# Kernel optimization log

Hardware: AMD Instinct MI355X
Metric: run time of the kernel (lower is better)

Reference implementation:

```python
import jax, jax.numpy as jnp
import numpy as np
from jax import lax

B, C, T, H, W = 4, 3, 2, 64, 64
DIM, HEADS, DH, MLP, DEPTH, SR, RES = 192, 3, 64, 768, 2, 2, 64
INNER = HEADS * DH  # 192 == DIM
N = RES * RES + 1   # 4097 tokens (cls + patches)


def setup_inputs() -> dict:
    key = jax.random.key(0)
    ks = iter(jax.random.split(key, 64))
    def rn(shape, s=0.02):
        return jax.random.normal(next(ks), shape, jnp.float32) * s
    d = {}
    d["x"] = jax.random.normal(next(ks), (B, C, T, H, W), jnp.float32)
    # patch embed conv3d (kernel (1,1,1) since patch_size=1) + layernorm
    d["pe_w"] = rn((DIM, C, 1, 1, 1))
    d["pe_b"] = jnp.zeros((DIM,), jnp.float32)
    d["pe_ln_g"] = jnp.ones((DIM,), jnp.float32)
    d["pe_ln_b"] = jnp.zeros((DIM,), jnp.float32)
    d["pos_emb"] = rn((1, T, N, DIM), 1.0)      # torch.randn
    d["space_token"] = rn((1, 1, DIM), 1.0)     # torch.randn
    ones2 = jnp.ones((DEPTH, DIM), jnp.float32)
    zeros2 = jnp.zeros((DEPTH, DIM), jnp.float32)
    # space transformer (Sattention with SR conv)
    d["s_ln1_g"], d["s_ln1_b"] = ones2, zeros2
    d["s_wq"] = rn((DEPTH, INNER, DIM))
    d["s_wkv"] = rn((DEPTH, 2 * INNER, DIM))
    d["s_wo"] = rn((DEPTH, DIM, INNER))
    d["s_bo"] = jnp.zeros((DEPTH, DIM), jnp.float32)
    d["s_sr_w"] = rn((DEPTH, DIM, DIM, SR, SR))
    d["s_sr_b"] = jnp.zeros((DEPTH, DIM), jnp.float32)
    d["s_ln2_g"], d["s_ln2_b"] = ones2, zeros2
    d["s_w1"] = rn((DEPTH, MLP, DIM))
    d["s_b1"] = jnp.zeros((DEPTH, MLP), jnp.float32)
    d["s_w2"] = rn((DEPTH, DIM, MLP))
    d["s_b2"] = jnp.zeros((DEPTH, DIM), jnp.float32)
    d["s_lnf_g"] = jnp.ones((DIM,), jnp.float32)
    d["s_lnf_b"] = jnp.zeros((DIM,), jnp.float32)
    # temporal transformer (plain attention over t=2 cls tokens)
    d["t_ln1_g"], d["t_ln1_b"] = ones2, zeros2
    d["t_wqkv"] = rn((DEPTH, 3 * INNER, DIM))
    d["t_wo"] = rn((DEPTH, DIM, INNER))
    d["t_bo"] = jnp.zeros((DEPTH, DIM), jnp.float32)
    d["t_ln2_g"], d["t_ln2_b"] = ones2, zeros2
    d["t_w1"] = rn((DEPTH, MLP, DIM))
    d["t_b1"] = jnp.zeros((DEPTH, MLP), jnp.float32)
    d["t_w2"] = rn((DEPTH, DIM, MLP))
    d["t_b2"] = jnp.zeros((DEPTH, DIM), jnp.float32)
    d["t_lnf_g"] = jnp.ones((DIM,), jnp.float32)
    d["t_lnf_b"] = jnp.zeros((DIM,), jnp.float32)
    return d


def _ln(x, g, b, eps=1e-5):
    m = jnp.mean(x, -1, keepdims=True)
    v = jnp.var(x, -1, keepdims=True)
    return (x - m) * lax.rsqrt(v + eps) * g + b


def _heads(t):
    b, n, _ = t.shape
    return t.reshape(b, n, HEADS, DH).transpose(0, 2, 1, 3)  # b h n d


def _attend(q, k, v):
    dots = jnp.einsum('bhid,bhjd->bhij', q, k) * (DH ** -0.5)
    attn = jax.nn.softmax(dots, axis=-1)
    o = jnp.einsum('bhij,bhjd->bhid', attn, v)
    return o.transpose(0, 2, 1, 3).reshape(q.shape[0], q.shape[2], INNER)


def _ff(x, w1, b1, w2, b2):
    h = jax.nn.gelu(x @ w1.T + b1, approximate=False)
    return h @ w2.T + b2


def _sattn(x, wq, wkv, wo, bo, srw, srb):
    bn = x.shape[0]
    q = _heads(x @ wq.T)
    # spatial reduction of non-cls tokens: b n d -> b d h w, conv stride SR
    xs = x[:, 1:].transpose(0, 2, 1).reshape(bn, DIM, RES, RES)
    xs = lax.conv_general_dilated(xs, srw, (SR, SR), 'VALID',
                                  dimension_numbers=('NCHW', 'OIHW', 'NCHW'))
    xs = xs + srb[None, :, None, None]
    xs = xs.reshape(bn, DIM, -1).transpose(0, 2, 1)
    xk = jnp.concatenate([x[:, :1], xs], axis=1)   # prepend cls token
    kv = xk @ wkv.T
    k, v = _heads(kv[..., :INNER]), _heads(kv[..., INNER:])
    return _attend(q, k, v) @ wo.T + bo


def _attn(x, wqkv, wo, bo):
    qkv = x @ wqkv.T
    q = _heads(qkv[..., :INNER])
    k = _heads(qkv[..., INNER:2 * INNER])
    v = _heads(qkv[..., 2 * INNER:])
    return _attend(q, k, v) @ wo.T + bo


def reference(x, pe_w, pe_b, pe_ln_g, pe_ln_b, pos_emb, space_token,
              s_ln1_g, s_ln1_b, s_wq, s_wkv, s_wo, s_bo, s_sr_w, s_sr_b,
              s_ln2_g, s_ln2_b, s_w1, s_b1, s_w2, s_b2, s_lnf_g, s_lnf_b,
              t_ln1_g, t_ln1_b, t_wqkv, t_wo, t_bo, t_ln2_g, t_ln2_b,
              t_w1, t_b1, t_w2, t_b2, t_lnf_g, t_lnf_b):
    # patch embed: (b,c,t,h,w) -> (b,t,hw,dim) with layernorm
    y = lax.conv_general_dilated(x, pe_w, (1, 1, 1), 'VALID',
                                 dimension_numbers=('NCDHW', 'OIDHW', 'NCDHW'))
    y = y + pe_b[None, :, None, None, None]
    y = jnp.transpose(y, (0, 2, 3, 4, 1)).reshape(B, T, RES * RES, DIM)
    y = _ln(y, pe_ln_g, pe_ln_b)
    cls = jnp.broadcast_to(space_token[:, None], (B, T, 1, DIM))
    xx = jnp.concatenate([cls, y], axis=2) + pos_emb[:, :, :N]
    xx = xx.reshape(B * T, N, DIM)
    for i in range(DEPTH):
        xx = _sattn(_ln(xx, s_ln1_g[i], s_ln1_b[i]), s_wq[i], s_wkv[i],
                    s_wo[i], s_bo[i], s_sr_w[i], s_sr_b[i]) + xx
        xx = _ff(_ln(xx, s_ln2_g[i], s_ln2_b[i]), s_w1[i], s_b1[i],
                 s_w2[i], s_b2[i]) + xx
    xx = _ln(xx, s_lnf_g, s_lnf_b)
    out = xx[:, 1:].reshape(B, T, RES, RES, DIM)
    z = xx[:, 0].reshape(B, T, DIM)
    for i in range(DEPTH):
        z = _attn(_ln(z, t_ln1_g[i], t_ln1_b[i]), t_wqkv[i], t_wo[i], t_bo[i]) + z
        z = _ff(_ln(z, t_ln2_g[i], t_ln2_b[i]), t_w1[i], t_b1[i], t_w2[i], t_b2[i]) + z
    z = _ln(z, t_lnf_g, t_lnf_b)
    return out + out * z[:, :, None, None, :]
```

## Files before the change

kernel.cpp:

```cpp
#include <hip/hip_runtime.h>
#include <hip/hip_bf16.h>
#include <math.h>

typedef __hip_bfloat16 bf16;
typedef short bf16x8 __attribute__((ext_vector_type(8)));
typedef float f32x4  __attribute__((ext_vector_type(4)));

#define BATCH 4
#define TT 2
#define BT 8
#define DIM 192
#define NTOK 4097
#define NKTOK 1025
#define HEADS 3
#define DH 64
#define MLPD 768
#define RES 64

__device__ __forceinline__ float b2f(bf16 v) { return __bfloat162float(v); }

__device__ __forceinline__ float rload(const void* p, size_t i, int flag) {
    if (flag) return __bfloat162float(((const bf16*)p)[i]);
    return ((const float*)p)[i];
}

__device__ __forceinline__ void unpack8(uint4 u, float* f) {
    unsigned w[4] = {u.x, u.y, u.z, u.w};
    #pragma unroll
    for (int k = 0; k < 4; ++k) {
        union { unsigned u; float f; } a, b;
        a.u = (w[k] & 0xFFFFu) << 16;
        b.u = w[k] & 0xFFFF0000u;
        f[2 * k] = a.f;
        f[2 * k + 1] = b.f;
    }
}

__device__ __forceinline__ void wload8(const void* W, size_t i, int flag, float* f) {
    if (flag) {
        uint4 u = *reinterpret_cast<const uint4*>((const bf16*)W + i);
        unpack8(u, f);
    } else {
        const float* p = (const float*)W + i;
        #pragma unroll
        for (int j = 0; j < 8; ++j) f[j] = p[j];
    }
}

__global__ void detect_kernel(const void* probe, int* flag) {
    unsigned u = *(const unsigned*)probe;
    *flag = (u == 0x3F800000u) ? 0 : 1;
}

__global__ __launch_bounds__(256) void patch_embed4_kernel(
        const void* __restrict__ x, const void* __restrict__ pe_w,
        const void* __restrict__ pe_b, const void* __restrict__ lng,
        const void* __restrict__ lnb, const void* __restrict__ pos,
        const void* __restrict__ st, float* __restrict__ XX,
        const int* __restrict__ dflag) {
    int flag = *dflag;
    int w = threadIdx.x >> 6, lane = threadIdx.x & 63;
    int row = blockIdx.x * 4 + w;
    int bt = row / NTOK, n = row % NTOK;
    int b = bt >> 1, t = bt & 1;
    int d0 = lane, d1 = lane + 64, d2 = lane + 128;
    float o0, o1, o2;
    if (n == 0) {
        o0 = rload(st, d0, flag); o1 = rload(st, d1, flag); o2 = rload(st, d2, flag);
    } else {
        int p = n - 1, hh = p >> 6, ww = p & 63;
        size_t base = (size_t)(b * 6 + t) * 4096 + hh * 64 + ww;
        float xv0 = rload(x, base, flag);
        float xv1 = rload(x, base + (size_t)TT * 4096, flag);
        float xv2 = rload(x, base + (size_t)2 * TT * 4096, flag);
        float c0 = rload(pe_b, d0, flag) + xv0 * rload(pe_w, d0 * 3, flag)
                 + xv1 * rload(pe_w, d0 * 3 + 1, flag) + xv2 * rload(pe_w, d0 * 3 + 2, flag);
        float c1 = rload(pe_b, d1, flag) + xv0 * rload(pe_w, d1 * 3, flag)
                 + xv1 * rload(pe_w, d1 * 3 + 1, flag) + xv2 * rload(pe_w, d1 * 3 + 2, flag);
        float c2 = rload(pe_b, d2, flag) + xv0 * rload(pe_w, d2 * 3, flag)
                 + xv1 * rload(pe_w, d2 * 3 + 1, flag) + xv2 * rload(pe_w, d2 * 3 + 2, flag);
        float s = c0 + c1 + c2;
        #pragma unroll
        for (int m = 32; m > 0; m >>= 1) s += __shfl_xor(s, m, 64);
        float mean = s * (1.f / 192.f);
        float e0 = c0 - mean, e1 = c1 - mean, e2 = c2 - mean;
        float s2 = e0 * e0 + e1 * e1 + e2 * e2;
        #pragma unroll
        for (int m = 32; m > 0; m >>= 1) s2 += __shfl_xor(s2, m, 64);
        float inv = rsqrtf(s2 * (1.f / 192.f) + 1e-5f);
        o0 = e0 * inv * rload(lng, d0, flag) + rload(lnb, d0, flag);
        o1 = e1 * inv * rload(lng, d1, flag) + rload(lnb, d1, flag);
        o2 = e2 * inv * rload(lng, d2, flag) + rload(lnb, d2, flag);
    }
    size_t pbase = ((size_t)t * NTOK + n) * DIM;
    o0 += rload(pos, pbase + d0, flag);
    o1 += rload(pos, pbase + d1, flag);
    o2 += rload(pos, pbase + d2, flag);
    float* xp = XX + (size_t)row * DIM;
    xp[d0] = o0; xp[d1] = o1; xp[d2] = o2;
}

__global__ __launch_bounds__(256) void ln4_kernel(const float* __restrict__ X,
        const void* __restrict__ g, const void* __restrict__ b, size_t goff,
        bf16* __restrict__ Y, const int* __restrict__ dflag) {
    int flag = *dflag;
    int w = threadIdx.x >> 6, lane = threadIdx.x & 63;
    size_t row = (size_t)blockIdx.x * 4 + w;
    const float* xp = X + row * DIM;
    float v0 = xp[lane], v1 = xp[lane + 64], v2 = xp[lane + 128];
    float s = v0 + v1 + v2;
    #pragma unroll
    for (int m = 32; m > 0; m >>= 1) s += __shfl_xor(s, m, 64);
    float mean = s * (1.f / 192.f);
    float e0 = v0 - mean, e1 = v1 - mean, e2 = v2 - mean;
    float s2 = e0 * e0 + e1 * e1 + e2 * e2;
    #pragma unroll
    for (int m = 32; m > 0; m >>= 1) s2 += __shfl_xor(s2, m, 64);
    float inv = rsqrtf(s2 * (1.f / 192.f) + 1e-5f);
    bf16* yp = Y + row * DIM;
    yp[lane]       = __float2bfloat16(e0 * inv * rload(g, goff + lane, flag)       + rload(b, goff + lane, flag));
    yp[lane + 64]  = __float2bfloat16(e1 * inv * rload(g, goff + lane + 64, flag)  + rload(b, goff + lane + 64, flag));
    yp[lane + 128] = __float2bfloat16(e2 * inv * rload(g, goff + lane + 128, flag) + rload(b, goff + lane + 128, flag));
}

__global__ __launch_bounds__(256) void gemm_mfma_kernel(
        const bf16* __restrict__ A, const void* __restrict__ W, size_t woff,
        const void* __restrict__ bias, size_t boff, const float* __restrict__ resid,
        float* __restrict__ Cf, bf16* __restrict__ Cb,
        int M, int N, int K, int do_gelu, const int* __restrict__ dflag) {
    __shared__ __align__(16) bf16 As[64 * 32];
    __shared__ __align__(16) bf16 Bs[64 * 32];
    int flag = *dflag;
    int tid = threadIdx.x;
    int wave = tid >> 6, lane = tid & 63;
    int quad = lane >> 4, l16 = lane & 15;
    int rowBase = blockIdx.y * 64;
    int colBase = blockIdx.x * 64;
    int srow = tid >> 2, scol = (tid & 3) * 8;

    f32x4 acc0 = {0.f, 0.f, 0.f, 0.f};
    f32x4 acc1 = acc0, acc2 = acc0, acc3 = acc0;

    for (int k0 = 0; k0 < K; k0 += 32) {
        {
            int gr = rowBase + srow;
            uint4 v = make_uint4(0u, 0u, 0u, 0u);
            if (gr < M) v = *reinterpret_cast<const uint4*>(A + (size_t)gr * K + k0 + scol);
            *reinterpret_cast<uint4*>(&As[srow * 32 + scol]) = v;
        }
        {
            int gr = colBase + srow;
            if (flag) {
                uint4 v = *reinterpret_cast<const uint4*>((const bf16*)W + woff + (size_t)gr * K + k0 + scol);
                *reinterpret_cast<uint4*>(&Bs[srow * 32 + scol]) = v;
            } else {
                const float* wp = (const float*)W + woff + (size_t)gr * K + k0 + scol;
                bf16 tmp8[8];
                #pragma unroll
                for (int j = 0; j < 8; ++j) tmp8[j] = __float2bfloat16(wp[j]);
                *reinterpret_cast<uint4*>(&Bs[srow * 32 + scol]) = *reinterpret_cast<uint4*>(tmp8);
            }
        }
        __syncthreads();
        bf16x8 af = *reinterpret_cast<bf16x8*>(&As[(wave * 16 + l16) * 32 + quad * 8]);
        bf16x8 bf0 = *reinterpret_cast<bf16x8*>(&Bs[(0 * 16 + l16) * 32 + quad * 8]);
        bf16x8 bf1 = *reinterpret_cast<bf16x8*>(&Bs[(1 * 16 + l16) * 32 + quad * 8]);
        bf16x8 bf2 = *reinterpret_cast<bf16x8*>(&Bs[(2 * 16 + l16) * 32 + quad * 8]);
        bf16x8 bf3 = *reinterpret_cast<bf16x8*>(&Bs[(3 * 16 + l16) * 32 + quad * 8]);
        acc0 = __builtin_amdgcn_mfma_f32_16x16x32_bf16(af, bf0, acc0, 0, 0, 0);
        acc1 = __builtin_amdgcn_mfma_f32_16x16x32_bf16(af, bf1, acc1, 0, 0, 0);
        acc2 = __builtin_amdgcn_mfma_f32_16x16x32_bf16(af, bf2, acc2, 0, 0, 0);
        acc3 = __builtin_amdgcn_mfma_f32_16x16x32_bf16(af, bf3, acc3, 0, 0, 0);
        __syncthreads();
    }

    f32x4 accs[4] = {acc0, acc1, acc2, acc3};
    #pragma unroll
    for (int t = 0; t < 4; ++t) {
        int col = colBase + t * 16 + l16;
        float bv = bias ? rload(bias, boff + col, flag) : 0.f;
        #pragma unroll
        for (int r = 0; r < 4; ++r) {
            int row = rowBase + wave * 16 + quad * 4 + r;
            if (row < M) {
                float v = accs[t][r] + bv;
                if (do_gelu) v = 0.5f * v * (1.f + erff(v * 0.70710678118654752f));
                if (resid) v += resid[(size_t)row * N + col];
                if (Cf) Cf[(size_t)row * N + col] = v;
                else    Cb[(size_t)row * N + col] = __float2bfloat16(v);
            }
        }
    }
}

__global__ void copy_cls_kernel(const bf16* __restrict__ AB, bf16* __restrict__ XK) {
    int bt = blockIdx.x, d = threadIdx.x;
    XK[(size_t)bt * NKTOK * DIM + d] = AB[(size_t)bt * NTOK * DIM + d];
}

__global__ void wtrans_kernel(const void* __restrict__ srw, bf16* __restrict__ WT,
                              const int* __restrict__ dflag) {
    int flag = *dflag;
    int idx = blockIdx.x * 256 + threadIdx.x;
    int i = idx / (192 * 768);
    int rem = idx - i * (192 * 768);
    int dout = rem / 768;
    int kp = rem - dout * 768;
    int q = kp / 192, c = kp - q * 192;
    size_t src = ((size_t)(i * 192 + dout) * 192 + c) * 4 + q;
    WT[idx] = __float2bfloat16(rload(srw, src, flag));
}

__global__ __launch_bounds__(256) void srconv_mfma_kernel(
        const bf16* __restrict__ XLN, const bf16* __restrict__ WT, size_t woff,
        const void* __restrict__ bias, size_t boff, bf16* __restrict__ XK,
        const int* __restrict__ dflag) {
    __shared__ __align__(16) bf16 As[64 * 32];
    __shared__ __align__(16) bf16 Bs[64 * 32];
    int flag = *dflag;
    int tid = threadIdx.x;
    int wave = tid >> 6, lane = tid & 63;
    int quad = lane >> 4, l16 = lane & 15;
    int rowBase = blockIdx.y * 64;
    int colBase = blockIdx.x * 64;
    int srow = tid >> 2, scol = (tid & 3) * 8;

    int arow = rowBase + srow;
    int abt = arow >> 10, apos = arow & 1023;
    int aoh = apos >> 5, aow = apos & 31;

    f32x4 acc0 = {0.f, 0.f, 0.f, 0.f};
    f32x4 acc1 = acc0, acc2 = acc0, acc3 = acc0;

    for (int k0 = 0; k0 < 768; k0 += 32) {
        int q = k0 / 192, c0 = k0 - q * 192;
        int kh = q >> 1, kw = q & 1;
        int n = 1 + ((2 * aoh + kh) << 6) + (2 * aow + kw);
        {
            uint4 v = *reinterpret_cast<const uint4*>(
                XLN + ((size_t)abt * NTOK + n) * DIM + c0 + scol);
            *reinterpret_cast<uint4*>(&As[srow * 32 + scol]) = v;
        }
        {
            int gr = colBase + srow;
            uint4 v = *reinterpret_cast<const uint4*>(WT + woff + (size_t)gr * 768 + k0 + scol);
            *reinterpret_cast<uint4*>(&Bs[srow * 32 + scol]) = v;
        }
        __syncthreads();
        bf16x8 af = *reinterpret_cast<bf16x8*>(&As[(wave * 16 + l16) * 32 + quad * 8]);
        bf16x8 bf0 = *reinterpret_cast<bf16x8*>(&Bs[(0 * 16 + l16) * 32 + quad * 8]);
        bf16x8 bf1 = *reinterpret_cast<bf16x8*>(&Bs[(1 * 16 + l16) * 32 + quad * 8]);
        bf16x8 bf2 = *reinterpret_cast<bf16x8*>(&Bs[(2 * 16 + l16) * 32 + quad * 8]);
        bf16x8 bf3 = *reinterpret_cast<bf16x8*>(&Bs[(3 * 16 + l16) * 32 + quad * 8]);
        acc0 = __builtin_amdgcn_mfma_f32_16x16x32_bf16(af, bf0, acc0, 0, 0, 0);
        acc1 = __builtin_amdgcn_mfma_f32_16x16x32_bf16(af, bf1, acc1, 0, 0, 0);
        acc2 = __builtin_amdgcn_mfma_f32_16x16x32_bf16(af, bf2, acc2, 0, 0, 0);
        acc3 = __builtin_amdgcn_mfma_f32_16x16x32_bf16(af, bf3, acc3, 0, 0, 0);
        __syncthreads();
    }

    f32x4 accs[4] = {acc0, acc1, acc2, acc3};
    #pragma unroll
    for (int t = 0; t < 4; ++t) {
        int col = colBase + t * 16 + l16;
        float bv = rload(bias, boff + col, flag);
        #pragma unroll
        for (int r = 0; r < 4; ++r) {
            int row = rowBase + wave * 16 + quad * 4 + r;
            int bt = row >> 10, pos = row & 1023;
            XK[((size_t)bt * NKTOK + 1 + pos) * DIM + col] = __float2bfloat16(accs[t][r] + bv);
        }
    }
}

__global__ __launch_bounds__(256) void sattn_mfma_kernel(const bf16* __restrict__ Q,
                                                         const bf16* __restrict__ KV,
                                                         bf16* __restrict__ O) {
    __shared__ __align__(16) bf16 Ks[32 * 72];
    __shared__ __align__(16) bf16 Vts[64 * 36];
    __shared__ __align__(16) bf16 Ps[4][16 * 68];

    int bt = blockIdx.x / HEADS, h = blockIdx.x % HEADS;
    int q0 = blockIdx.y * 64;
    int tid = threadIdx.x;
    int wave = tid >> 6, lane = tid & 63;
    int quad = lane >> 4, l16 = lane & 15;

    int qrow = q0 + wave * 16 + l16;
    int qr = (qrow < NTOK) ? qrow : (NTOK - 1);
    const bf16* qp = Q + ((size_t)bt * NTOK + qr) * DIM + h * DH + quad * 8;
    bf16x8 aq0 = *reinterpret_cast<const bf16x8*>(qp);
    bf16x8 aq1 = *reinterpret_cast<const bf16x8*>(qp + 32);

    float l_r[4] = {0.f, 0.f, 0.f, 0.f};
    f32x4 O0 = {0.f, 0.f, 0.f, 0.f}, O1 = O0, O2 = O0, O3 = O0;

    int skey = tid & 31, sdh0 = (tid >> 5) * 8;
    union U8 { bf16x8 v; uint2 u[2]; };

    for (int kt0 = 0; kt0 < NKTOK; kt0 += 32) {
        __syncthreads();
        {
            int gkey = kt0 + skey;
            uint4 kv4 = make_uint4(0u, 0u, 0u, 0u), vv4 = make_uint4(0u, 0u, 0u, 0u);
            if (gkey < NKTOK) {
                const bf16* kp = KV + ((size_t)bt * NKTOK + gkey) * (2 * DIM) + h * DH + sdh0;
                kv4 = *reinterpret_cast<const uint4*>(kp);
                vv4 = *reinterpret_cast<const uint4*>(kp + DIM);
            }
            *reinterpret_cast<uint2*>(&Ks[skey * 72 + sdh0])     = make_uint2(kv4.x, kv4.y);
            *reinterpret_cast<uint2*>(&Ks[skey * 72 + sdh0 + 4]) = make_uint2(kv4.z, kv4.w);
            const bf16* vb = reinterpret_cast<const bf16*>(&vv4);
            #pragma unroll
            for (int j = 0; j < 8; ++j) Vts[(sdh0 + j) * 36 + skey] = vb[j];
        }
        __syncthreads();

        f32x4 S[2];
        #pragma unroll
        for (int sub = 0; sub < 2; ++sub) {
            U8 k0c, k1c;
            const bf16* kr = &Ks[(sub * 16 + l16) * 72 + quad * 8];
            k0c.u[0] = *reinterpret_cast<const uint2*>(kr);
            k0c.u[1] = *reinterpret_cast<const uint2*>(kr + 4);
            const bf16* kr2 = kr + 32;
            k1c.u[0] = *reinterpret_cast<const uint2*>(kr2);
            k1c.u[1] = *reinterpret_cast<const uint2*>(kr2 + 4);
            f32x4 z = {0.f, 0.f, 0.f, 0.f};
            z = __builtin_amdgcn_mfma_f32_16x16x32_bf16(aq0, k0c.v, z, 0, 0, 0);
            z = __builtin_amdgcn_mfma_f32_16x16x32_bf16(aq1, k1c.v, z, 0, 0, 0);
            S[sub] = z;
        }

        bool oob0 = (kt0 + l16) >= NKTOK;
        bool oob1 = (kt0 + 16 + l16) >= NKTOK;
        #pragma unroll
        for (int r = 0; r < 4; ++r) {
            float p0 = oob0 ? 0.f : __expf(S[0][r] * 0.125f);
            float p1 = oob1 ? 0.f : __expf(S[1][r] * 0.125f);
            l_r[r] += p0 + p1;
            Ps[wave][(quad * 4 + r) * 68 + l16]      = __float2bfloat16(p0);
            Ps[wave][(quad * 4 + r) * 68 + 16 + l16] = __float2bfloat16(p1);
        }

        U8 pa;
        const bf16* pp = &Ps[wave][l16 * 68 + quad * 8];
        pa.u[0] = *reinterpret_cast<const uint2*>(pp);
        pa.u[1] = *reinterpret_cast<const uint2*>(pp + 4);
        U8 vf[4];
        #pragma unroll
        for (int t = 0; t < 4; ++t) {
            const bf16* vp = &Vts[(t * 16 + l16) * 36 + quad * 8];
            vf[t].u[0] = *reinterpret_cast<const uint2*>(vp);
            vf[t].u[1] = *reinterpret_cast<const uint2*>(vp + 4);
        }
        O0 = __builtin_amdgcn_mfma_f32_16x16x32_bf16(pa.v, vf[0].v, O0, 0, 0, 0);
        O1 = __builtin_amdgcn_mfma_f32_16x16x32_bf16(pa.v, vf[1].v, O1, 0, 0, 0);
        O2 = __builtin_amdgcn_mfma_f32_16x16x32_bf16(pa.v, vf[2].v, O2, 0, 0, 0);
        O3 = __builtin_amdgcn_mfma_f32_16x16x32_bf16(pa.v, vf[3].v, O3, 0, 0, 0);
    }

    #pragma unroll
    for (int r = 0; r < 4; ++r) {
        #pragma unroll
        for (int msk = 1; msk < 16; msk <<= 1)
            l_r[r] += __shfl_xor(l_r[r], msk, 64);
    }

    f32x4 Os[4] = {O0, O1, O2, O3};
    #pragma unroll
    for (int r = 0; r < 4; ++r) {
        int row = q0 + wave * 16 + quad * 4 + r;
        if (row < NTOK) {
            float inv = 1.f / l_r[r];
            bf16* op = O + ((size_t)bt * NTOK + row) * DIM + h * DH + l16;
            #pragma unroll
            for (int t = 0; t < 4; ++t)
                op[t * 16] = __float2bfloat16(Os[t][r] * inv);
        }
    }
}

__global__ __launch_bounds__(256) void temporal_fused_kernel(
        const float* __restrict__ XX,
        const void* lnf_g, const void* lnf_b,
        const void* ln1_g, const void* ln1_b, const void* wqkv,
        const void* wo, const void* bo, const void* ln2_g, const void* ln2_b,
        const void* w1, const void* b1, const void* w2, const void* b2,
        const void* tlnf_g, const void* tlnf_b,
        float* __restrict__ ZF, const int* __restrict__ dflag) {
    __shared__ float Zs[8 * 192];
    __shared__ float B1[8 * 192];
    __shared__ float B2[8 * 768];
    __shared__ float Sc[12][4];
    int flag = *dflag;
    int tid = threadIdx.x;
    int g = tid >> 5, l32 = tid & 31;

    auto ln_row = [&](const float* src, long stride, float* dst, const void* gg,
                      const void* bb, size_t goff) {
        const float* xp = src + (size_t)g * stride;
        float v[6];
        float s = 0.f;
        #pragma unroll
        for (int j = 0; j < 6; ++j) { v[j] = xp[l32 + 32 * j]; s += v[j]; }
        #pragma unroll
        for (int m = 16; m > 0; m >>= 1) s += __shfl_xor(s, m, 32);
        float mean = s * (1.f / 192.f);
        float s2 = 0.f;
        #pragma unroll
        for (int j = 0; j < 6; ++j) { float dv = v[j] - mean; s2 += dv * dv; }
        #pragma unroll
        for (int m = 16; m > 0; m >>= 1) s2 += __shfl_xor(s2, m, 32);
        float inv = rsqrtf(s2 * (1.f / 192.f) + 1e-5f);
        #pragma unroll
        for (int j = 0; j < 6; ++j) {
            int d = l32 + 32 * j;
            dst[g * 192 + d] = (v[j] - mean) * inv * rload(gg, goff + d, flag)
                               + rload(bb, goff + d, flag);
        }
    };

    ln_row(XX, (long)NTOK * DIM, Zs, lnf_g, lnf_b, 0);
    __syncthreads();

    for (int i = 0; i < 2; ++i) {
        size_t oLN   = (size_t)i * DIM;
        size_t oWQKV = (size_t)i * 3 * DIM * DIM;
        size_t oWO   = (size_t)i * DIM * DIM;
        size_t oW1   = (size_t)i * MLPD * DIM;
        size_t oB1   = (size_t)i * MLPD;
        size_t oW2   = (size_t)i * DIM * MLPD;

        ln_row(Zs, 192, B1, ln1_g, ln1_b, oLN);
        __syncthreads();

        for (int n = tid; n < 576; n += 256) {
            float acc[8] = {0.f, 0.f, 0.f, 0.f, 0.f, 0.f, 0.f, 0.f};
            for (int k = 0; k < 192; k += 8) {
                float wf[8];
                wload8(wqkv, oWQKV + (size_t)n * 192 + k, flag, wf);
                #pragma unroll
                for (int j = 0; j < 8; ++j)
                    #pragma unroll
                    for (int r = 0; r < 8; ++r)
                        acc[r] += B1[r * 192 + k + j] * wf[j];
            }
            #pragma unroll
            for (int r = 0; r < 8; ++r) B2[r * 576 + n] = acc[r];
        }
        __syncthreads();

        if (tid < 12) {
            int b = tid / 3, h = tid % 3;
            int r0 = 2 * b, r1 = r0 + 1;
            float s00 = 0.f, s01 = 0.f, s10 = 0.f, s11 = 0.f;
            for (int d = 0; d < 64; ++d) {
                float q0 = B2[r0 * 576 + h * 64 + d];
                float q1 = B2[r1 * 576 + h * 64 + d];
                float k0 = B2[r0 * 576 + 192 + h * 64 + d];
                float k1 = B2[r1 * 576 + 192 + h * 64 + d];
                s00 += q0 * k0; s01 += q0 * k1; s10 += q1 * k0; s11 += q1 * k1;
            }
            Sc[tid][0] = s00 * 0.125f; Sc[tid][1] = s01 * 0.125f;
            Sc[tid][2] = s10 * 0.125f; Sc[tid][3] = s11 * 0.125f;
        }
        __syncthreads();

        for (int idx = tid; idx < 768; idx += 256) {
            int p = idx >> 6, d = idx & 63;
            int b = p / 3, h = p % 3;
            int r0 = 2 * b, r1 = r0 + 1;
            float s00 = Sc[p][0], s01 = Sc[p][1], s10 = Sc[p][2], s11 = Sc[p][3];
            float m0 = fmaxf(s00, s01), m1 = fmaxf(s10, s11);
            float e00 = __expf(s00 - m0), e01 = __expf(s01 - m0);
            float e10 = __expf(s10 - m1), e11 = __expf(s11 - m1);
            float i0 = 1.f / (e00 + e01), i1 = 1.f / (e10 + e11);
            float v0 = B2[r0 * 576 + 384 + h * 64 + d];
            float v1 = B2[r1 * 576 + 384 + h * 64 + d];
            B1[r0 * 192 + h * 64 + d] = (e00 * v0 + e01 * v1) * i0;
            B1[r1 * 192 + h * 64 + d] = (e10 * v0 + e11 * v1) * i1;
        }
        __syncthreads();

        if (tid < 192) {
            int n = tid;
            float bv = rload(bo, oLN + n, flag);
            float acc[8] = {bv, bv, bv, bv, bv, bv, bv, bv};
            for (int k = 0; k < 192; k += 8) {
                float wf[8];
                wload8(wo, oWO + (size_t)n * 192 + k, flag, wf);
                #pragma unroll
                for (int j = 0; j < 8; ++j)
                    #pragma unroll
                    for (int r = 0; r < 8; ++r)
                        acc[r] += B1[r * 192 + k + j] * wf[j];
            }
            #pragma unroll
            for (int r = 0; r < 8; ++r) Zs[r * 192 + n] += acc[r];
        }
        __syncthreads();

        ln_row(Zs, 192, B1, ln2_g, ln2_b, oLN);
        __syncthreads();

        for (int n = tid; n < 768; n += 256) {
            float bv = rload(b1, oB1 + n, flag);
            float acc[8] = {bv, bv, bv, bv, bv, bv, bv, bv};
            for (int k = 0; k < 192; k += 8) {
                float wf[8];
                wload8(w1, oW1 + (size_t)n * 192 + k, flag, wf);
                #pragma unroll
                for (int j = 0; j < 8; ++j)
                    #pragma unroll
                    for (int r = 0; r < 8; ++r)
                        acc[r] += B1[r * 192 + k + j] * wf[j];
            }
            #pragma unroll
            for (int r = 0; r < 8; ++r) {
                float v = acc[r];
                B2[r * 768 + n] = 0.5f * v * (1.f + erff(v * 0.70710678118654752f));
            }
        }
        __syncthreads();

        if (tid < 192) {
            int n = tid;
            float bv = rload(b2, oLN + n, flag);
            float acc[8] = {bv, bv, bv, bv, bv, bv, bv, bv};
            for (int k = 0; k < 768; k += 8) {
                float wf[8];
                wload8(w2, oW2 + (size_t)n * 768 + k, flag, wf);
                #pragma unroll
                for (int j = 0; j < 8; ++j)
                    #pragma unroll
                    for (int r = 0; r < 8; ++r)
                        acc[r] += B2[r * 768 + k + j] * wf[j];
            }
            #pragma unroll
            for (int r = 0; r < 8; ++r) Zs[r * 192 + n] += acc[r];
        }
        __syncthreads();
    }

    ln_row(Zs, 192, B1, tlnf_g, tlnf_b, 0);
    __syncthreads();
    for (int idx = tid; idx < 8 * 192; idx += 256) ZF[idx] = B1[idx];
}

__global__ __launch_bounds__(256) void final4_kernel(const float* __restrict__ XX,
        const void* __restrict__ g, const void* __restrict__ b,
        const float* __restrict__ ZF, void* __restrict__ out,
        const int* __restrict__ dflag) {
    int flag = *dflag;
    int w = threadIdx.x >> 6, lane = threadIdx.x & 63;
    int tok = blockIdx.x * 4 + w;
    int bt = tok >> 12, p = tok & 4095;
    size_t row = (size_t)bt * NTOK + 1 + p;
    const float* xp = XX + row * DIM;
    float v0 = xp[lane], v1 = xp[lane + 64], v2 = xp[lane + 128];
    float s = v0 + v1 + v2;
    #pragma unroll
    for (int m = 32; m > 0; m >>= 1) s += __shfl_xor(s, m, 64);
    float mean = s * (1.f / 192.f);
    float e0 = v0 - mean, e1 = v1 - mean, e2 = v2 - mean;
    float s2 = e0 * e0 + e1 * e1 + e2 * e2;
    #pragma unroll
    for (int m = 32; m > 0; m >>= 1) s2 += __shfl_xor(s2, m, 64);
    float inv = rsqrtf(s2 * (1.f / 192.f) + 1e-5f);
    const float* zp = ZF + bt * DIM;
    float o0 = (e0 * inv * rload(g, lane, flag)       + rload(b, lane, flag))       * (1.f + zp[lane]);
    float o1 = (e1 * inv * rload(g, lane + 64, flag)  + rload(b, lane + 64, flag))  * (1.f + zp[lane + 64]);
    float o2 = (e2 * inv * rload(g, lane + 128, flag) + rload(b, lane + 128, flag)) * (1.f + zp[lane + 128]);
    size_t ob = (size_t)tok * DIM;
    if (flag) {
        bf16* op = (bf16*)out + ob;
        op[lane] = __float2bfloat16(o0);
        op[lane + 64] = __float2bfloat16(o1);
        op[lane + 128] = __float2bfloat16(o2);
    } else {
        float* op = (float*)out + ob;
        op[lane] = o0; op[lane + 64] = o1; op[lane + 128] = o2;
    }
}

extern "C" void kernel_launch(void* const* d_in, const int* in_sizes, int n_in,
                              void* d_out, int out_size, void* d_ws, size_t ws_size,
                              hipStream_t stream) {
    const void* x       = d_in[0];
    const void* pe_w    = d_in[1];
    const void* pe_b    = d_in[2];
    const void* pe_ln_g = d_in[3];
    const void* pe_ln_b = d_in[4];
    const void* pos_emb = d_in[5];
    const void* space_t = d_in[6];
    const void* s_ln1_g = d_in[7];
    const void* s_ln1_b = d_in[8];
    const void* s_wq    = d_in[9];
    const void* s_wkv   = d_in[10];
    const void* s_wo    = d_in[11];
    const void* s_bo    = d_in[12];
    const void* s_sr_w  = d_in[13];
    const void* s_sr_b  = d_in[14];
    const void* s_ln2_g = d_in[15];
    const void* s_ln2_b = d_in[16];
    const void* s_w1    = d_in[17];
    const void* s_b1    = d_in[18];
    const void* s_w2    = d_in[19];
    const void* s_b2    = d_in[20];
    const void* s_lnf_g = d_in[21];
    const void* s_lnf_b = d_in[22];
    const void* t_ln1_g = d_in[23];
    const void* t_ln1_b = d_in[24];
    const void* t_wqkv  = d_in[25];
    const void* t_wo    = d_in[26];
    const void* t_bo    = d_in[27];
    const void* t_ln2_g = d_in[28];
    const void* t_ln2_b = d_in[29];
    const void* t_w1    = d_in[30];
    const void* t_b1    = d_in[31];
    const void* t_w2    = d_in[32];
    const void* t_b2    = d_in[33];
    const void* t_lnf_g = d_in[34];
    const void* t_lnf_b = d_in[35];

    const int M  = BT * NTOK;
    const int MK = BT * NKTOK;
    const int CHROWS = 8194;

    char* base = (char*)d_ws;
    int* dflag = (int*)base;
    size_t off = 256;
    auto carve = [&](size_t bytes) -> void* {
        void* p = base + off;
        off += (bytes + 255) & ~(size_t)255;
        return p;
    };
    float* XX = (float*)carve((size_t)M * DIM * 4);
    bf16*  AB = (bf16*) carve((size_t)M * DIM * 2);
    bf16*  QH = (bf16*) carve((size_t)M * DIM * 2);
    bf16*  XK = (bf16*) carve((size_t)MK * DIM * 2);
    bf16*  KV = (bf16*) carve((size_t)MK * 2 * DIM * 2);
    bf16*  WT = (bf16*) carve((size_t)2 * DIM * 768 * 2);
    float* ZF = (float*)carve(BT * DIM * 4);

    detect_kernel<<<1, 1, 0, stream>>>(pe_ln_g, dflag);
    wtrans_kernel<<<(2 * 192 * 768) / 256, 256, 0, stream>>>(s_sr_w, WT, dflag);
    patch_embed4_kernel<<<M / 4, 256, 0, stream>>>(x, pe_w, pe_b, pe_ln_g, pe_ln_b,
                                                   pos_emb, space_t, XX, dflag);

    for (int i = 0; i < 2; ++i) {
        size_t oLN  = (size_t)i * DIM;
        size_t oWQ  = (size_t)i * DIM * DIM;
        size_t oWKV = (size_t)i * 2 * DIM * DIM;
        size_t oWO  = (size_t)i * DIM * DIM;
        size_t oWT  = (size_t)i * DIM * 768;
        size_t oW1  = (size_t)i * MLPD * DIM;
        size_t oB1  = (size_t)i * MLPD;
        size_t oW2  = (size_t)i * DIM * MLPD;

        ln4_kernel<<<M / 4, 256, 0, stream>>>(XX, s_ln1_g, s_ln1_b, oLN, AB, dflag);
        gemm_mfma_kernel<<<dim3(DIM / 64, (M + 63) / 64), 256, 0, stream>>>(
            AB, s_wq, oWQ, nullptr, 0, nullptr, nullptr, QH, M, DIM, DIM, 0, dflag);
        copy_cls_kernel<<<BT, DIM, 0, stream>>>(AB, XK);
        srconv_mfma_kernel<<<dim3(DIM / 64, (BT * 1024) / 64), 256, 0, stream>>>(
            AB, WT, oWT, s_sr_b, oLN, XK, dflag);
        gemm_mfma_kernel<<<dim3(2 * DIM / 64, (MK + 63) / 64), 256, 0, stream>>>(
            XK, s_wkv, oWKV, nullptr, 0, nullptr, nullptr, KV, MK, 2 * DIM, DIM, 0, dflag);
        sattn_mfma_kernel<<<dim3(BT * HEADS, (NTOK + 63) / 64), 256, 0, stream>>>(QH, KV, AB);
        gemm_mfma_kernel<<<dim3(DIM / 64, (M + 63) / 64), 256, 0, stream>>>(
            AB, s_wo, oWO, s_bo, oLN, XX, XX, nullptr, M, DIM, DIM, 0, dflag);
        ln4_kernel<<<M / 4, 256, 0, stream>>>(XX, s_ln2_g, s_ln2_b, oLN, AB, dflag);
        for (int c = 0; c < 4; ++c) {
            size_t aoff = (size_t)c * CHROWS * DIM;
            gemm_mfma_kernel<<<dim3(MLPD / 64, (CHROWS + 63) / 64), 256, 0, stream>>>(
                AB + aoff, s_w1, oW1, s_b1, oB1, nullptr, nullptr, QH, CHROWS, MLPD, DIM, 1, dflag);
            gemm_mfma_kernel<<<dim3(DIM / 64, (CHROWS + 63) / 64), 256, 0, stream>>>(
                QH, s_w2, oW2, s_b2, oLN, XX + aoff, XX + aoff, nullptr, CHROWS, DIM, MLPD, 0, dflag);
        }
    }

    temporal_fused_kernel<<<1, 256, 0, stream>>>(
        XX, s_lnf_g, s_lnf_b, t_ln1_g, t_ln1_b, t_wqkv, t_wo, t_bo,
        t_ln2_g, t_ln2_b, t_w1, t_b1, t_w2, t_b2, t_lnf_g, t_lnf_b, ZF, dflag);

    final4_kernel<<<(BT * 4096) / 4, 256, 0, stream>>>(XX, s_lnf_g, s_lnf_b, ZF, d_out, dflag);
}
```

Baseline: 1.110 ms.

## Parallelize temporal transformer across batches and split-K its small GEMVs

The single-block temporal kernel becomes four blocks of 1024 threads, one per batch element, each handling its two time-step rows. The output projection and the second MLP layer now split K across four thread groups and reduce the partial sums in shared memory. This is meant to shorten the serial latency of this tiny tail kernel. In exchange each weight matrix is read from global memory by four blocks instead of one.

```diff
diff --git a/kernel.cpp b/kernel.cpp
--- a/kernel.cpp
+++ b/kernel.cpp
@@ -381,7 +381,7 @@
     }
 }
 
-__global__ __launch_bounds__(256) void temporal_fused_kernel(
+__global__ __launch_bounds__(1024) void temporal_fused_kernel(
         const float* __restrict__ XX,
         const void* lnf_g, const void* lnf_b,
         const void* ln1_g, const void* ln1_b, const void* wqkv,
@@ -389,39 +389,34 @@
         const void* w1, const void* b1, const void* w2, const void* b2,
         const void* tlnf_g, const void* tlnf_b,
         float* __restrict__ ZF, const int* __restrict__ dflag) {
-    __shared__ float Zs[8 * 192];
-    __shared__ float B1[8 * 192];
-    __shared__ float B2[8 * 768];
-    __shared__ float Sc[12][4];
+    __shared__ float Zs[2 * 192];
+    __shared__ float B1s[2 * 192];
+    __shared__ float B2s[2 * 768];
+    __shared__ float Sc[3][4];
+    __shared__ float Part[4][192][2];
     int flag = *dflag;
+    int bb = blockIdx.x;
     int tid = threadIdx.x;
-    int g = tid >> 5, l32 = tid & 31;
-
-    auto ln_row = [&](const float* src, long stride, float* dst, const void* gg,
-                      const void* bb, size_t goff) {
-        const float* xp = src + (size_t)g * stride;
-        float v[6];
-        float s = 0.f;
-        #pragma unroll
-        for (int j = 0; j < 6; ++j) { v[j] = xp[l32 + 32 * j]; s += v[j]; }
-        #pragma unroll
-        for (int m = 16; m > 0; m >>= 1) s += __shfl_xor(s, m, 32);
+    int w = tid >> 6, lane = tid & 63;
+
+    auto ln_row = [&](const float* xp, float* dst, const void* gg, const void* bbp, size_t goff) {
+        float v0 = xp[lane], v1 = xp[lane + 64], v2 = xp[lane + 128];
+        float s = v0 + v1 + v2;
+        #pragma unroll
+        for (int m = 32; m > 0; m >>= 1) s += __shfl_xor(s, m, 64);
         float mean = s * (1.f / 192.f);
-        float s2 = 0.f;
-        #pragma unroll
-        for (int j = 0; j < 6; ++j) { float dv = v[j] - mean; s2 += dv * dv; }
-        #pragma unroll
-        for (int m = 16; m > 0; m >>= 1) s2 += __shfl_xor(s2, m, 32);
+        float e0 = v0 - mean, e1 = v1 - mean, e2 = v2 - mean;
+        float s2 = e0 * e0 + e1 * e1 + e2 * e2;
+        #pragma unroll
+        for (int m = 32; m > 0; m >>= 1) s2 += __shfl_xor(s2, m, 64);
         float inv = rsqrtf(s2 * (1.f / 192.f) + 1e-5f);
-        #pragma unroll
-        for (int j = 0; j < 6; ++j) {
-            int d = l32 + 32 * j;
-            dst[g * 192 + d] = (v[j] - mean) * inv * rload(gg, goff + d, flag)
-                               + rload(bb, goff + d, flag);
-        }
+        dst[lane]       = e0 * inv * rload(gg, goff + lane, flag)       + rload(bbp, goff + lane, flag);
+        dst[lane + 64]  = e1 * inv * rload(gg, goff + lane + 64, flag)  + rload(bbp, goff + lane + 64, flag);
+        dst[lane + 128] = e2 * inv * rload(gg, goff + lane + 128, flag) + rload(bbp, goff + lane + 128, flag);
     };
 
-    ln_row(XX, (long)NTOK * DIM, Zs, lnf_g, lnf_b, 0);
+    if (w < 2)
+        ln_row(XX + (size_t)(2 * bb + w) * NTOK * DIM, Zs + w * 192, lnf_g, lnf_b, 0);
     __syncthreads();
 
     for (int i = 0; i < 2; ++i) {
@@ -432,120 +427,126 @@
         size_t oB1   = (size_t)i * MLPD;
         size_t oW2   = (size_t)i * DIM * MLPD;
 
-        ln_row(Zs, 192, B1, ln1_g, ln1_b, oLN);
-        __syncthreads();
-
-        for (int n = tid; n < 576; n += 256) {
-            float acc[8] = {0.f, 0.f, 0.f, 0.f, 0.f, 0.f, 0.f, 0.f};
+        if (w < 2) ln_row(Zs + w * 192, B1s + w * 192, ln1_g, ln1_b, oLN);
+        __syncthreads();
+
+        if (tid < 576) {
+            int n = tid;
+            float a0 = 0.f, a1 = 0.f;
+            #pragma unroll 6
             for (int k = 0; k < 192; k += 8) {
                 float wf[8];
                 wload8(wqkv, oWQKV + (size_t)n * 192 + k, flag, wf);
                 #pragma unroll
-                for (int j = 0; j < 8; ++j)
-                    #pragma unroll
-                    for (int r = 0; r < 8; ++r)
-                        acc[r] += B1[r * 192 + k + j] * wf[j];
-            }
-            #pragma unroll
-            for (int r = 0; r < 8; ++r) B2[r * 576 + n] = acc[r];
-        }
-        __syncthreads();
-
-        if (tid < 12) {
-            int b = tid / 3, h = tid % 3;
-            int r0 = 2 * b, r1 = r0 + 1;
+                for (int j = 0; j < 8; ++j) {
+                    a0 += B1s[k + j] * wf[j];
+                    a1 += B1s[192 + k + j] * wf[j];
+                }
+            }
+            B2s[n] = a0; B2s[576 + n] = a1;
+        }
+        __syncthreads();
+
+        if (tid < 3) {
+            int h = tid;
             float s00 = 0.f, s01 = 0.f, s10 = 0.f, s11 = 0.f;
             for (int d = 0; d < 64; ++d) {
-                float q0 = B2[r0 * 576 + h * 64 + d];
-                float q1 = B2[r1 * 576 + h * 64 + d];
-                float k0 = B2[r0 * 576 + 192 + h * 64 + d];
-                float k1 = B2[r1 * 576 + 192 + h * 64 + d];
+                float q0 = B2s[h * 64 + d];
+                float q1 = B2s[576 + h * 64 + d];
+                float k0 = B2s[192 + h * 64 + d];
+                float k1 = B2s[576 + 192 + h * 64 + d];
                 s00 += q0 * k0; s01 += q0 * k1; s10 += q1 * k0; s11 += q1 * k1;
             }
-            Sc[tid][0] = s00 * 0.125f; Sc[tid][1] = s01 * 0.125f;
-            Sc[tid][2] = s10 * 0.125f; Sc[tid][3] = s11 * 0.125f;
-        }
-        __syncthreads();
-
-        for (int idx = tid; idx < 768; idx += 256) {
-            int p = idx >> 6, d = idx & 63;
-            int b = p / 3, h = p % 3;
-            int r0 = 2 * b, r1 = r0 + 1;
-            float s00 = Sc[p][0], s01 = Sc[p][1], s10 = Sc[p][2], s11 = Sc[p][3];
+            Sc[h][0] = s00 * 0.125f; Sc[h][1] = s01 * 0.125f;
+            Sc[h][2] = s10 * 0.125f; Sc[h][3] = s11 * 0.125f;
+        }
+        __syncthreads();
+
+        if (tid < 192) {
+            int h = tid >> 6, d = tid & 63;
+            float s00 = Sc[h][0], s01 = Sc[h][1], s10 = Sc[h][2], s11 = Sc[h][3];
             float m0 = fmaxf(s00, s01), m1 = fmaxf(s10, s11);
             float e00 = __expf(s00 - m0), e01 = __expf(s01 - m0);
             float e10 = __expf(s10 - m1), e11 = __expf(s11 - m1);
             float i0 = 1.f / (e00 + e01), i1 = 1.f / (e10 + e11);
-            float v0 = B2[r0 * 576 + 384 + h * 64 + d];
-            float v1 = B2[r1 * 576 + 384 + h * 64 + d];
-            B1[r0 * 192 + h * 64 + d] = (e00 * v0 + e01 * v1) * i0;
-            B1[r1 * 192 + h * 64 + d] = (e10 * v0 + e11 * v1) * i1;
-        }
-        __syncthreads();
-
-        if (tid < 192) {
-            int n = tid;
-            float bv = rload(bo, oLN + n, flag);
-            float acc[8] = {bv, bv, bv, bv, bv, bv, bv, bv};
-            for (int k = 0; k < 192; k += 8) {
+            float v0 = B2s[384 + h * 64 + d];
+            float v1 = B2s[576 + 384 + h * 64 + d];
+            B1s[h * 64 + d]       = (e00 * v0 + e01 * v1) * i0;
+            B1s[192 + h * 64 + d] = (e10 * v0 + e11 * v1) * i1;
+        }
+        __syncthreads();
+
+        if (tid < 768) {
+            int ks = tid / 192, n = tid - ks * 192;
+            float a0 = 0.f, a1 = 0.f;
+            #pragma unroll 3
+            for (int k = ks * 48; k < ks * 48 + 48; k += 8) {
                 float wf[8];
                 wload8(wo, oWO + (size_t)n * 192 + k, flag, wf);
                 #pragma unroll
-                for (int j = 0; j < 8; ++j)
-                    #pragma unroll
-                    for (int r = 0; r < 8; ++r)
-                        acc[r] += B1[r * 192 + k + j] * wf[j];
-            }
-            #pragma unroll
-            for (int r = 0; r < 8; ++r) Zs[r * 192 + n] += acc[r];
-        }
-        __syncthreads();
-
-        ln_row(Zs, 192, B1, ln2_g, ln2_b, oLN);
-        __syncthreads();
-
-        for (int n = tid; n < 768; n += 256) {
+                for (int j = 0; j < 8; ++j) {
+                    a0 += B1s[k + j] * wf[j];
+                    a1 += B1s[192 + k + j] * wf[j];
+                }
+            }
+            Part[ks][n][0] = a0; Part[ks][n][1] = a1;
+        }
+        __syncthreads();
+        if (tid < 192) {
+            float bv = rload(bo, oLN + tid, flag);
+            Zs[tid]       += bv + Part[0][tid][0] + Part[1][tid][0] + Part[2][tid][0] + Part[3][tid][0];
+            Zs[192 + tid] += bv + Part[0][tid][1] + Part[1][tid][1] + Part[2][tid][1] + Part[3][tid][1];
+        }
+        __syncthreads();
+
+        if (w < 2) ln_row(Zs + w * 192, B1s + w * 192, ln2_g, ln2_b, oLN);
+        __syncthreads();
+
+        if (tid < 768) {
+            int n = tid;
             float bv = rload(b1, oB1 + n, flag);
-            float acc[8] = {bv, bv, bv, bv, bv, bv, bv, bv};
+            float a0 = bv, a1 = bv;
+            #pragma unroll 6
             for (int k = 0; k < 192; k += 8) {
                 float wf[8];
                 wload8(w1, oW1 + (size_t)n * 192 + k, flag, wf);
                 #pragma unroll
-                for (int j = 0; j < 8; ++j)
-                    #pragma unroll
-                    for (int r = 0; r < 8; ++r)
-                        acc[r] += B1[r * 192 + k + j] * wf[j];
-            }
-            #pragma unroll
-            for (int r = 0; r < 8; ++r) {
-                float v = acc[r];
-                B2[r * 768 + n] = 0.5f * v * (1.f + erff(v * 0.70710678118654752f));
-            }
-        }
-        __syncthreads();
-
-        if (tid < 192) {
-            int n = tid;
-            float bv = rload(b2, oLN + n, flag);
-            float acc[8] = {bv, bv, bv, bv, bv, bv, bv, bv};
-            for (int k = 0; k < 768; k += 8) {
+                for (int j = 0; j < 8; ++j) {
+                    a0 += B1s[k + j] * wf[j];
+                    a1 += B1s[192 + k + j] * wf[j];
+                }
+            }
+            B2s[n]       = 0.5f * a0 * (1.f + erff(a0 * 0.70710678118654752f));
+            B2s[768 + n] = 0.5f * a1 * (1.f + erff(a1 * 0.70710678118654752f));
+        }
+        __syncthreads();
+
+        if (tid < 768) {
+            int ks = tid / 192, n = tid - ks * 192;
+            float a0 = 0.f, a1 = 0.f;
+            #pragma unroll 6
+            for (int k = ks * 192; k < ks * 192 + 192; k += 8) {
                 float wf[8];
                 wload8(w2, oW2 + (size_t)n * 768 + k, flag, wf);
                 #pragma unroll
-                for (int j = 0; j < 8; ++j)
-                    #pragma unroll
-                    for (int r = 0; r < 8; ++r)
-                        acc[r] += B2[r * 768 + k + j] * wf[j];
-            }
-            #pragma unroll
-            for (int r = 0; r < 8; ++r) Zs[r * 192 + n] += acc[r];
-        }
-        __syncthreads();
-    }
-
-    ln_row(Zs, 192, B1, tlnf_g, tlnf_b, 0);
-    __syncthreads();
-    for (int idx = tid; idx < 8 * 192; idx += 256) ZF[idx] = B1[idx];
+                for (int j = 0; j < 8; ++j) {
+                    a0 += B2s[k + j] * wf[j];
+                    a1 += B2s[768 + k + j] * wf[j];
+                }
+            }
+            Part[ks][n][0] = a0; Part[ks][n][1] = a1;
+        }
+        __syncthreads();
+        if (tid < 192) {
+            float bv = rload(b2, oLN + tid, flag);
+            Zs[tid]       += bv + Part[0][tid][0] + Part[1][tid][0] + Part[2][tid][0] + Part[3][tid][0];
+            Zs[192 + tid] += bv + Part[0][tid][1] + Part[1][tid][1] + Part[2][tid][1] + Part[3][tid][1];
+        }
+        __syncthreads();
+    }
+
+    if (w < 2)
+        ln_row(Zs + w * 192, ZF + (size_t)(2 * bb + w) * 192, tlnf_g, tlnf_b, 0);
 }
 
 __global__ __launch_bounds__(256) void final4_kernel(const float* __restrict__ XX,
@@ -680,7 +681,7 @@
         }
     }
 
-    temporal_fused_kernel<<<1, 256, 0, stream>>>(
+    temporal_fused_kernel<<<4, 1024, 0, stream>>>(
         XX, s_lnf_g, s_lnf_b, t_ln1_g, t_ln1_b, t_wqkv, t_wo, t_bo,
         t_ln2_g, t_ln2_b, t_w1, t_b1, t_w2, t_b2, t_lnf_g, t_lnf_b, ZF, dflag);
 
```

New measurement: 1.189 ms. 7.1% more time.
